# Optimization experiments

Hardware: AMD Instinct MI355X
Metric: run time of the kernel (lower is better)

The kernel has to match this reference:

```python
import jax, jax.numpy as jnp
import numpy as np

NEG = -100000000.0  # NOT_POSSIBLE_TRANSITION
B, T, F, NT = 64, 512, 1024, 50
H = NT + 2  # +2 for start/stop tags
START, STOP = H - 2, H - 1


def setup_inputs() -> dict:
    key = jax.random.key(0)
    k0, k1, k2, k3 = jax.random.split(key, 4)
    features = jax.random.normal(k0, (B, T, F), jnp.float32)
    tags = jax.random.randint(k1, (B, T), 0, NT)
    masks = jnp.ones((B, T), jnp.float32)
    W = jax.random.normal(k2, (H, F), jnp.float32) * 0.02  # nn.Linear weight
    b = jnp.zeros((H,), jnp.float32)                        # nn.Linear bias
    transition = jax.random.normal(k3, (H, H), jnp.float32)
    transition = transition.at[START, :].set(NEG).at[:, STOP].set(NEG)
    return dict(features=features, W=W, b=b, transition=transition,
                masks=masks, tags=tags)


def _forward_algorithm(emit, masks, transition):
    # emit: [B,T,H], masks: [B,T]
    b_, _, h = emit.shape
    init = jnp.full((b_, h), NEG, emit.dtype).at[:, START].set(0.0)

    def step(scores, xs):
        emit_t, mask_t = xs  # [B,H], [B]
        # score_t[b, i] = logsumexp_j(scores[b,j] + transition[i,j] + emit_t[b,i])
        s = scores[:, None, :] + transition[None, :, :] + emit_t[:, :, None]
        s = jax.nn.logsumexp(s, axis=-1)
        m = mask_t[:, None]
        scores = s * m + scores * (1.0 - m)
        return scores, None

    scores, _ = jax.lax.scan(step, init, (emit.transpose(1, 0, 2), masks.T))
    return jax.nn.logsumexp(scores + transition[STOP], axis=-1)  # [B]


def _gold_score(emit, tags, masks, transition):
    b_ = emit.shape[0]
    emit_sc = jnp.take_along_axis(emit, tags[:, :, None], axis=2)[:, :, 0]  # [B,T]
    start = jnp.full((b_, 1), START, tags.dtype)
    tags_ext = jnp.concatenate([start, tags], axis=1)  # [B,T+1]
    trans_sc = transition[tags_ext[:, 1:], tags_ext[:, :-1]]  # [B,T]
    last_pos = masks.sum(axis=1).astype(jnp.int32)  # index into tags_ext
    last_tag = jnp.take_along_axis(tags_ext, last_pos[:, None], axis=1)[:, 0]
    last_score = transition[STOP, last_tag]
    return ((trans_sc + emit_sc) * masks).sum(axis=1) + last_score  # [B]


def reference(features, W, b, transition, masks, tags):
    emit = features @ W.T + b  # [B,T,H]
    fwd = _forward_algorithm(emit, masks, transition)
    gold = _gold_score(emit, tags, masks, transition)
    return (fwd - gold).mean()  # CRF NLL loss (scalar)


if __name__ == "__main__":
    print(reference(**setup_inputs()))
```

## Files before the change

### kernel.cpp

```cpp
#include <hip/hip_runtime.h>
#include <hip/hip_bf16.h>
#include <math.h>


#define NEGV   (-100000000.0f)
#define BB     64
#define TT     512
#define FF     1024
#define HH     52
#define HP     64
#define S_START 50
#define S_STOP  51
#define NCHUNK 8
#define CLEN   (TT / NCHUNK)

typedef __bf16 bf16x8 __attribute__((ext_vector_type(8)));
typedef __bf16 bf16x4 __attribute__((ext_vector_type(4)));
typedef float  f32x4  __attribute__((ext_vector_type(4)));

#define WS_EMIT   0u
#define WS_CHUNK  8388608u
#define WS_WBF    16777216u
#define WS_GOLD   16908288u
#define WS_CEXP   16908544u

__global__ __launch_bounds__(256) void k_prep(const float* __restrict__ W,
                                              __bf16* __restrict__ wbf) {
  int n = blockIdx.x;
  for (int k = threadIdx.x; k < FF; k += 256) {
    float v = (n < HH) ? W[n * FF + k] : 0.0f;
    wbf[n * FF + k] = (__bf16)v;
  }
}

__global__ __launch_bounds__(256) void k_emit(const float* __restrict__ feat,
                                              const __bf16* __restrict__ wbf,
                                              const float* __restrict__ bias,
                                              float* __restrict__ emit) {
  __shared__ __align__(16) __bf16 Asm[64 * 72];
  const int tid = threadIdx.x;
  const int wv = tid >> 6;
  const int l  = tid & 63;
  const int lm = l & 15;
  const int q  = l >> 4;
  const size_t row0 = (size_t)blockIdx.x * 64;

  float bn[4];
#pragma unroll
  for (int nt = 0; nt < 4; ++nt) {
    int n = nt * 16 + lm;
    bn[nt] = (n < HH) ? bias[n] : 0.0f;
  }

  f32x4 acc[4] = {};

  const int srow = tid >> 4;
  const int scol = (tid & 15) * 4;

  for (int kc = 0; kc < 16; ++kc) {
    const int k0 = kc * 64;
    if (kc) __syncthreads();
#pragma unroll
    for (int p = 0; p < 4; ++p) {
      int r = srow + p * 16;
      f32x4 v = *(const f32x4*)(feat + (row0 + r) * FF + k0 + scol);
      bf16x4 bv;
#pragma unroll
      for (int j = 0; j < 4; ++j) bv[j] = (__bf16)v[j];
      *(bf16x4*)&Asm[r * 72 + scol] = bv;
    }
    __syncthreads();
#pragma unroll
    for (int kk = 0; kk < 2; ++kk) {
      bf16x8 af = *(const bf16x8*)&Asm[(wv * 16 + lm) * 72 + kk * 32 + q * 8];
#pragma unroll
      for (int nt = 0; nt < 4; ++nt) {
        bf16x8 bfr = *(const bf16x8*)(wbf + (size_t)(nt * 16 + lm) * FF + k0 + kk * 32 + q * 8);
        acc[nt] = __builtin_amdgcn_mfma_f32_16x16x32_bf16(af, bfr, acc[nt], 0, 0, 0);
      }
    }
  }

#pragma unroll
  for (int nt = 0; nt < 4; ++nt) {
#pragma unroll
    for (int rr = 0; rr < 4; ++rr) {
      size_t m = row0 + wv * 16 + q * 4 + rr;
      emit[m * HP + nt * 16 + lm] = acc[nt][rr] + bn[nt];
    }
  }
}

__global__ __launch_bounds__(256) void k_gold(const float* __restrict__ emit,
                                              const int* __restrict__ tags,
                                              const float* __restrict__ masks,
                                              const float* __restrict__ trans,
                                              float* __restrict__ gold) {
  const int b = blockIdx.x;
  const int tid = threadIdx.x;
  float acc = 0.f, msum = 0.f;
  for (int t = tid; t < TT; t += 256) {
    int tg = tags[b * TT + t];
    int pv = (t == 0) ? S_START : tags[b * TT + t - 1];
    float m = masks[b * TT + t];
    float e = emit[((size_t)b * TT + t) * HP + tg];
    float tr = trans[tg * HH + pv];
    acc += (e + tr) * m;
    msum += m;
  }
#pragma unroll
  for (int d = 32; d > 0; d >>= 1) {
    acc += __shfl_xor(acc, d);
    msum += __shfl_xor(msum, d);
  }
  __shared__ float ra[4], rm[4];
  if ((tid & 63) == 0) { ra[tid >> 6] = acc; rm[tid >> 6] = msum; }
  __syncthreads();
  if (tid == 0) {
    float tot = ra[0] + ra[1] + ra[2] + ra[3];
    float ms  = rm[0] + rm[1] + rm[2] + rm[3];
    int lp = (int)(ms + 0.5f);
    int lt = (lp == 0) ? S_START : tags[b * TT + lp - 1];
    gold[b] = tot + trans[S_STOP * HH + lt];
  }
}

__global__ __launch_bounds__(256) void k_chunks(const float* __restrict__ emit,
                                                const float* __restrict__ trans,
                                                const float* __restrict__ masks,
                                                float* __restrict__ chunks,
                                                float* __restrict__ cexp) {
  const int blk = blockIdx.x;
  const int b = blk >> 3, c = blk & 7;
  const int tid = threadIdx.x;
  const int wv = tid >> 6;
  const int l = tid & 63;
  const int lm = l & 15;
  const int q = l >> 4;

  __shared__ __align__(16) __bf16 PT[2][64 * 72];
  __shared__ float wmax[2][4];

  const int m = wv * 16 + lm;
  bf16x8 afrag[2];
#pragma unroll
  for (int kk = 0; kk < 2; ++kk) {
#pragma unroll
    for (int j = 0; j < 8; ++j) {
      int k = kk * 32 + q * 8 + j;
      float tv;
      if (k >= HH) tv = NEGV;
      else if (m >= HH) tv = 0.0f;
      else tv = trans[m * HH + k];
      afrag[kk][j] = (__bf16)__expf(tv);
    }
  }

  for (int idx = tid; idx < 4096; idx += 256) {
    int n = idx >> 6, mm = idx & 63;
    PT[0][n * 72 + mm] = (__bf16)((n == mm) ? 1.0f : 0.0f);
  }
  if (tid < 4) wmax[0][tid] = 1.0f;
  __syncthreads();

  const float* eb = emit + ((size_t)b * TT + c * CLEN) * HP + wv * 16 + q * 4;
  const float* mb = masks + b * TT + c * CLEN;
  f32x4 epf = *(const f32x4*)(eb);
  float mpf = mb[0];

  int pb = 0;
  int eacc = 0;

  for (int t = 0; t < CLEN; ++t) {
    f32x4 ecur = epf;
    float mcur = mpf;
    int tn = (t + 1 < CLEN) ? t + 1 : t;
    epf = *(const f32x4*)(eb + (size_t)tn * HP);
    mpf = mb[tn];

    if (mcur != 0.0f) {
      float pm = fmaxf(fmaxf(wmax[pb][0], wmax[pb][1]),
                       fmaxf(wmax[pb][2], wmax[pb][3]));
      int r = ilogbf(pm);
      const int nb = pb ^ 1;

      f32x4 acc[4] = {};
#pragma unroll
      for (int kk = 0; kk < 2; ++kk) {
#pragma unroll
        for (int nt = 0; nt < 4; ++nt) {
          bf16x8 bfr = *(const bf16x8*)&PT[pb][(nt * 16 + lm) * 72 + kk * 32 + q * 8];
          acc[nt] = __builtin_amdgcn_mfma_f32_16x16x32_bf16(afrag[kk], bfr, acc[nt], 0, 0, 0);
        }
      }
      float s[4];
#pragma unroll
      for (int rr = 0; rr < 4; ++rr) s[rr] = ldexpf(__expf(ecur[rr]), -r);

      float mx = 0.0f;
#pragma unroll
      for (int nt = 0; nt < 4; ++nt) {
        bf16x4 w4;
#pragma unroll
        for (int rr = 0; rr < 4; ++rr) {
          float v = acc[nt][rr] * s[rr];
          mx = fmaxf(mx, v);
          w4[rr] = (__bf16)v;
        }
        *(bf16x4*)&PT[nb][(nt * 16 + lm) * 72 + wv * 16 + q * 4] = w4;
      }
#pragma unroll
      for (int d = 1; d < 64; d <<= 1) mx = fmaxf(mx, __shfl_xor(mx, d));
      if (l == 0) wmax[nb][wv] = mx;
      eacc += r;
      __syncthreads();
      pb = nb;
    }
  }

  for (int idx = tid; idx < 4096; idx += 256) {
    int i = idx >> 6, j = idx & 63;
    chunks[(size_t)blk * 4096 + idx] = (float)PT[pb][j * 72 + i];
  }
  if (tid == 0) cexp[blk] = (float)eacc;
}

__global__ __launch_bounds__(64) void k_combine(const float* __restrict__ chunks,
                                                const float* __restrict__ cexp,
                                                const float* __restrict__ trans,
                                                const float* __restrict__ gold,
                                                float* __restrict__ out) {
  const int b = blockIdx.x;
  const int l = threadIdx.x;
  __shared__ float vsh[64];
  float v = (l == S_START) ? 1.0f : 0.0f;
  float esum = 0.0f;
  const float LN2 = 0.6931471805599453f;

  for (int cc = 0; cc < NCHUNK; ++cc) {
    vsh[l] = v;
    __syncthreads();
    const f32x4* Mr = (const f32x4*)(chunks + ((size_t)b * NCHUNK + cc) * 4096 + l * 64);
    float u = 0.0f;
#pragma unroll
    for (int jj = 0; jj < 16; ++jj) {
      f32x4 mv = Mr[jj];
      u += mv[0] * vsh[jj * 4 + 0] + mv[1] * vsh[jj * 4 + 1] +
           mv[2] * vsh[jj * 4 + 2] + mv[3] * vsh[jj * 4 + 3];
    }
    esum += cexp[b * NCHUNK + cc] * LN2;
    float mxx = u;
#pragma unroll
    for (int d = 1; d < 64; d <<= 1) mxx = fmaxf(mxx, __shfl_xor(mxx, d));
    if (mxx > 0.0f) {
      int ee = ilogbf(mxx);
      u = ldexpf(u, -ee);
      esum += (float)ee * LN2;
    }
    v = u;
    __syncthreads();
  }

  float ts = (l < HH) ? trans[S_STOP * HH + l] : NEGV;
  float contrib = v * __expf(ts);
#pragma unroll
  for (int d = 1; d < 64; d <<= 1) contrib += __shfl_xor(contrib, d);
  if (l == 0) {
    float fwd = __logf(contrib) + esum;
    atomicAdd(out, (fwd - gold[b]) * (1.0f / 64.0f));
  }
}

extern "C" void kernel_launch(void* const* d_in, const int* in_sizes, int n_in,
                              void* d_out, int out_size, void* d_ws, size_t ws_size,
                              hipStream_t stream) {
  (void)in_sizes; (void)n_in; (void)out_size; (void)ws_size;
  const float* feat  = (const float*)d_in[0];
  const float* W     = (const float*)d_in[1];
  const float* bias  = (const float*)d_in[2];
  const float* trans = (const float*)d_in[3];
  const float* masks = (const float*)d_in[4];
  const int*   tags  = (const int*)d_in[5];

  char* ws = (char*)d_ws;
  float*  emit   = (float*)(ws + WS_EMIT);
  float*  chunks = (float*)(ws + WS_CHUNK);
  __bf16* wbf    = (__bf16*)(ws + WS_WBF);
  float*  gold   = (float*)(ws + WS_GOLD);
  float*  cexp   = (float*)(ws + WS_CEXP);

  hipMemsetAsync(d_out, 0, sizeof(float), stream);
  k_prep<<<HP, 256, 0, stream>>>(W, wbf);
  k_emit<<<(BB * TT) / 64, 256, 0, stream>>>(feat, wbf, bias, emit);
  k_gold<<<BB, 256, 0, stream>>>(emit, tags, masks, trans, gold);
  k_chunks<<<BB * NCHUNK, 256, 0, stream>>>(emit, trans, masks, chunks, cexp);
  k_combine<<<BB, 64, 0, stream>>>(chunks, cexp, trans, gold, (float*)d_out);
}
```

Measured before the change: 298.6 us.

## Run one CRF chunk per wavefront with fixed rescaling and register-staged emit GEMM

The chunked forward-algorithm kernel now gives each wavefront a whole 64x64 chunk product, with sixteen chunks per sequence instead of eight. This removes the per-step block barrier and the shared-memory max exchange. Rescaling uses a fixed shift plus a max check every eight steps, so the cross-wave reduction no longer runs on every step. The emission GEMM loads features straight into registers with a one-step prefetch instead of staging them through LDS, and the combine kernel reads chunk matrices in a coalesced layout. The risks are bf16 overflow or underflow between the sparse rescale checks, higher register pressure, and more chunk data to combine.

```diff
diff --git a/kernel.cpp b/kernel.cpp
--- a/kernel.cpp
+++ b/kernel.cpp
@@ -11,8 +11,8 @@
 #define HP     64
 #define S_START 50
 #define S_STOP  51
-#define NCHUNK 8
-#define CLEN   (TT / NCHUNK)
+#define NCH    16
+#define CLEN   (TT / NCH)
 
 typedef __bf16 bf16x8 __attribute__((ext_vector_type(8)));
 typedef __bf16 bf16x4 __attribute__((ext_vector_type(4)));
@@ -20,9 +20,9 @@
 
 #define WS_EMIT   0u
 #define WS_CHUNK  8388608u
-#define WS_WBF    16777216u
-#define WS_GOLD   16908288u
-#define WS_CEXP   16908544u
+#define WS_WBF    25165824u
+#define WS_GOLD   25296896u
+#define WS_CEXP   25297152u
 
 __global__ __launch_bounds__(256) void k_prep(const float* __restrict__ W,
                                               __bf16* __restrict__ wbf) {
@@ -37,13 +37,13 @@
                                               const __bf16* __restrict__ wbf,
                                               const float* __restrict__ bias,
                                               float* __restrict__ emit) {
-  __shared__ __align__(16) __bf16 Asm[64 * 72];
   const int tid = threadIdx.x;
   const int wv = tid >> 6;
   const int l  = tid & 63;
   const int lm = l & 15;
   const int q  = l >> 4;
   const size_t row0 = (size_t)blockIdx.x * 64;
+  const float* fr = feat + (row0 + wv * 16 + lm) * FF;
 
   float bn[4];
 #pragma unroll
@@ -54,31 +54,44 @@
 
   f32x4 acc[4] = {};
 
-  const int srow = tid >> 4;
-  const int scol = (tid & 15) * 4;
+  f32x4 xa[2][2];
+#pragma unroll
+  for (int kk = 0; kk < 2; ++kk)
+#pragma unroll
+    for (int h = 0; h < 2; ++h)
+      xa[kk][h] = *(const f32x4*)(fr + kk * 32 + q * 8 + h * 4);
 
   for (int kc = 0; kc < 16; ++kc) {
+    bf16x8 af[2];
+#pragma unroll
+    for (int kk = 0; kk < 2; ++kk)
+#pragma unroll
+      for (int j = 0; j < 4; ++j) {
+        af[kk][j]     = (__bf16)xa[kk][0][j];
+        af[kk][4 + j] = (__bf16)xa[kk][1][j];
+      }
+    f32x4 xn[2][2];
+    if (kc < 15) {
+      const float* nf = fr + (kc + 1) * 64;
+#pragma unroll
+      for (int kk = 0; kk < 2; ++kk)
+#pragma unroll
+        for (int h = 0; h < 2; ++h)
+          xn[kk][h] = *(const f32x4*)(nf + kk * 32 + q * 8 + h * 4);
+    }
     const int k0 = kc * 64;
-    if (kc) __syncthreads();
-#pragma unroll
-    for (int p = 0; p < 4; ++p) {
-      int r = srow + p * 16;
-      f32x4 v = *(const f32x4*)(feat + (row0 + r) * FF + k0 + scol);
-      bf16x4 bv;
-#pragma unroll
-      for (int j = 0; j < 4; ++j) bv[j] = (__bf16)v[j];
-      *(bf16x4*)&Asm[r * 72 + scol] = bv;
-    }
-    __syncthreads();
-#pragma unroll
-    for (int kk = 0; kk < 2; ++kk) {
-      bf16x8 af = *(const bf16x8*)&Asm[(wv * 16 + lm) * 72 + kk * 32 + q * 8];
+#pragma unroll
+    for (int kk = 0; kk < 2; ++kk)
 #pragma unroll
       for (int nt = 0; nt < 4; ++nt) {
         bf16x8 bfr = *(const bf16x8*)(wbf + (size_t)(nt * 16 + lm) * FF + k0 + kk * 32 + q * 8);
-        acc[nt] = __builtin_amdgcn_mfma_f32_16x16x32_bf16(af, bfr, acc[nt], 0, 0, 0);
-      }
-    }
+        acc[nt] = __builtin_amdgcn_mfma_f32_16x16x32_bf16(af[kk], bfr, acc[nt], 0, 0, 0);
+      }
+#pragma unroll
+    for (int kk = 0; kk < 2; ++kk)
+#pragma unroll
+      for (int h = 0; h < 2; ++h)
+        xa[kk][h] = xn[kk][h];
   }
 
 #pragma unroll
@@ -125,104 +138,111 @@
   }
 }
 
-__global__ __launch_bounds__(256) void k_chunks(const float* __restrict__ emit,
-                                                const float* __restrict__ trans,
-                                                const float* __restrict__ masks,
-                                                float* __restrict__ chunks,
-                                                float* __restrict__ cexp) {
-  const int blk = blockIdx.x;
-  const int b = blk >> 3, c = blk & 7;
+__global__ __launch_bounds__(256, 1) void k_chunks(const float* __restrict__ emit,
+                                                   const float* __restrict__ trans,
+                                                   const float* __restrict__ masks,
+                                                   float* __restrict__ chunks,
+                                                   float* __restrict__ cexp) {
   const int tid = threadIdx.x;
   const int wv = tid >> 6;
-  const int l = tid & 63;
+  const int l  = tid & 63;
   const int lm = l & 15;
-  const int q = l >> 4;
-
-  __shared__ __align__(16) __bf16 PT[2][64 * 72];
-  __shared__ float wmax[2][4];
-
-  const int m = wv * 16 + lm;
-  bf16x8 afrag[2];
-#pragma unroll
-  for (int kk = 0; kk < 2; ++kk) {
-#pragma unroll
-    for (int j = 0; j < 8; ++j) {
-      int k = kk * 32 + q * 8 + j;
-      float tv;
-      if (k >= HH) tv = NEGV;
-      else if (m >= HH) tv = 0.0f;
-      else tv = trans[m * HH + k];
-      afrag[kk][j] = (__bf16)__expf(tv);
-    }
-  }
-
-  for (int idx = tid; idx < 4096; idx += 256) {
+  const int q  = l >> 4;
+  const int chunk = blockIdx.x * 4 + wv;
+  const int b = chunk >> 4, c = chunk & 15;
+
+  __shared__ __align__(16) __bf16 PTall[4][64 * 72];
+  __bf16* pt = PTall[wv];
+
+  bf16x8 afrag[4][2];
+#pragma unroll
+  for (int mt = 0; mt < 4; ++mt)
+#pragma unroll
+    for (int kk = 0; kk < 2; ++kk)
+#pragma unroll
+      for (int j = 0; j < 8; ++j) {
+        int m = mt * 16 + lm, k = kk * 32 + q * 8 + j;
+        float tv = (k >= HH) ? NEGV : ((m >= HH) ? 0.0f : trans[m * HH + k]);
+        afrag[mt][kk][j] = (__bf16)__expf(tv);
+      }
+
+  for (int idx = l; idx < 4096; idx += 64) {
     int n = idx >> 6, mm = idx & 63;
-    PT[0][n * 72 + mm] = (__bf16)((n == mm) ? 1.0f : 0.0f);
-  }
-  if (tid < 4) wmax[0][tid] = 1.0f;
-  __syncthreads();
-
-  const float* eb = emit + ((size_t)b * TT + c * CLEN) * HP + wv * 16 + q * 4;
+    pt[n * 72 + mm] = (__bf16)((n == mm) ? 1.0f : 0.0f);
+  }
+
+  const float* eb = emit + ((size_t)(b * TT + c * CLEN)) * HP;
   const float* mb = masks + b * TT + c * CLEN;
-  f32x4 epf = *(const f32x4*)(eb);
+
+  f32x4 ep[4];
+#pragma unroll
+  for (int mt = 0; mt < 4; ++mt) ep[mt] = *(const f32x4*)(eb + mt * 16 + q * 4);
   float mpf = mb[0];
 
-  int pb = 0;
-  int eacc = 0;
+  int eacc = 0, rpend = 0;
+  const float LOG2E = 1.4426950408889634f;
 
   for (int t = 0; t < CLEN; ++t) {
-    f32x4 ecur = epf;
+    f32x4 ec[4];
+#pragma unroll
+    for (int mt = 0; mt < 4; ++mt) ec[mt] = ep[mt];
     float mcur = mpf;
     int tn = (t + 1 < CLEN) ? t + 1 : t;
-    epf = *(const f32x4*)(eb + (size_t)tn * HP);
+#pragma unroll
+    for (int mt = 0; mt < 4; ++mt)
+      ep[mt] = *(const f32x4*)(eb + (size_t)tn * HP + mt * 16 + q * 4);
     mpf = mb[tn];
 
     if (mcur != 0.0f) {
-      float pm = fmaxf(fmaxf(wmax[pb][0], wmax[pb][1]),
-                       fmaxf(wmax[pb][2], wmax[pb][3]));
-      int r = ilogbf(pm);
-      const int nb = pb ^ 1;
-
-      f32x4 acc[4] = {};
-#pragma unroll
-      for (int kk = 0; kk < 2; ++kk) {
+      float sh = (float)(7 + rpend);
+      eacc += 7 + rpend;
+      rpend = 0;
+      float s[4][4];
+#pragma unroll
+      for (int mt = 0; mt < 4; ++mt)
+#pragma unroll
+        for (int rr = 0; rr < 4; ++rr)
+          s[mt][rr] = __builtin_amdgcn_exp2f(fmaf(ec[mt][rr], LOG2E, -sh));
+
+      bf16x8 bfr[2][4];
+#pragma unroll
+      for (int kk = 0; kk < 2; ++kk)
+#pragma unroll
+        for (int nt = 0; nt < 4; ++nt)
+          bfr[kk][nt] = *(const bf16x8*)&pt[(nt * 16 + lm) * 72 + kk * 32 + q * 8];
+
+      const bool trk = ((t & 7) == 7) && (t != CLEN - 1);
+      float lmax = 0.0f;
+      f32x4 zero = {};
+#pragma unroll
+      for (int mt = 0; mt < 4; ++mt) {
 #pragma unroll
         for (int nt = 0; nt < 4; ++nt) {
-          bf16x8 bfr = *(const bf16x8*)&PT[pb][(nt * 16 + lm) * 72 + kk * 32 + q * 8];
-          acc[nt] = __builtin_amdgcn_mfma_f32_16x16x32_bf16(afrag[kk], bfr, acc[nt], 0, 0, 0);
+          f32x4 a = __builtin_amdgcn_mfma_f32_16x16x32_bf16(afrag[mt][0], bfr[0][nt], zero, 0, 0, 0);
+          a = __builtin_amdgcn_mfma_f32_16x16x32_bf16(afrag[mt][1], bfr[1][nt], a, 0, 0, 0);
+          bf16x4 w4;
+#pragma unroll
+          for (int rr = 0; rr < 4; ++rr) {
+            float v = a[rr] * s[mt][rr];
+            if (trk) lmax = fmaxf(lmax, v);
+            w4[rr] = (__bf16)v;
+          }
+          *(bf16x4*)&pt[(nt * 16 + lm) * 72 + mt * 16 + q * 4] = w4;
         }
       }
-      float s[4];
-#pragma unroll
-      for (int rr = 0; rr < 4; ++rr) s[rr] = ldexpf(__expf(ecur[rr]), -r);
-
-      float mx = 0.0f;
-#pragma unroll
-      for (int nt = 0; nt < 4; ++nt) {
-        bf16x4 w4;
-#pragma unroll
-        for (int rr = 0; rr < 4; ++rr) {
-          float v = acc[nt][rr] * s[rr];
-          mx = fmaxf(mx, v);
-          w4[rr] = (__bf16)v;
-        }
-        *(bf16x4*)&PT[nb][(nt * 16 + lm) * 72 + wv * 16 + q * 4] = w4;
-      }
-#pragma unroll
-      for (int d = 1; d < 64; d <<= 1) mx = fmaxf(mx, __shfl_xor(mx, d));
-      if (l == 0) wmax[nb][wv] = mx;
-      eacc += r;
-      __syncthreads();
-      pb = nb;
-    }
-  }
-
-  for (int idx = tid; idx < 4096; idx += 256) {
-    int i = idx >> 6, j = idx & 63;
-    chunks[(size_t)blk * 4096 + idx] = (float)PT[pb][j * 72 + i];
-  }
-  if (tid == 0) cexp[blk] = (float)eacc;
+      if (trk) {
+#pragma unroll
+        for (int d = 1; d < 64; d <<= 1) lmax = fmaxf(lmax, __shfl_xor(lmax, d));
+        rpend = ilogbf(lmax);
+      }
+    }
+  }
+
+  for (int idx = l; idx < 4096; idx += 64) {
+    int jj = idx >> 8, i = (idx >> 2) & 63, jr = idx & 3;
+    chunks[(size_t)chunk * 4096 + idx] = (float)pt[(jj * 4 + jr) * 72 + i];
+  }
+  if (l == 0) cexp[chunk] = (float)eacc;
 }
 
 __global__ __launch_bounds__(64) void k_combine(const float* __restrict__ chunks,
@@ -237,18 +257,22 @@
   float esum = 0.0f;
   const float LN2 = 0.6931471805599453f;
 
-  for (int cc = 0; cc < NCHUNK; ++cc) {
+  for (int cc = 0; cc < NCH; ++cc) {
     vsh[l] = v;
     __syncthreads();
-    const f32x4* Mr = (const f32x4*)(chunks + ((size_t)b * NCHUNK + cc) * 4096 + l * 64);
-    float u = 0.0f;
+    const f32x4* M = (const f32x4*)(chunks + ((size_t)(b * NCH + cc)) * 4096);
+    f32x4 u4 = {};
 #pragma unroll
     for (int jj = 0; jj < 16; ++jj) {
-      f32x4 mv = Mr[jj];
-      u += mv[0] * vsh[jj * 4 + 0] + mv[1] * vsh[jj * 4 + 1] +
-           mv[2] * vsh[jj * 4 + 2] + mv[3] * vsh[jj * 4 + 3];
-    }
-    esum += cexp[b * NCHUNK + cc] * LN2;
+      f32x4 m4 = M[jj * 64 + l];
+      const float* vj = &vsh[jj * 4];
+      u4[0] += m4[0] * vj[0];
+      u4[1] += m4[1] * vj[1];
+      u4[2] += m4[2] * vj[2];
+      u4[3] += m4[3] * vj[3];
+    }
+    float u = (u4[0] + u4[1]) + (u4[2] + u4[3]);
+    esum += cexp[b * NCH + cc] * LN2;
     float mxx = u;
 #pragma unroll
     for (int d = 1; d < 64; d <<= 1) mxx = fmaxf(mxx, __shfl_xor(mxx, d));
@@ -293,6 +317,6 @@
   k_prep<<<HP, 256, 0, stream>>>(W, wbf);
   k_emit<<<(BB * TT) / 64, 256, 0, stream>>>(feat, wbf, bias, emit);
   k_gold<<<BB, 256, 0, stream>>>(emit, tags, masks, trans, gold);
-  k_chunks<<<BB * NCHUNK, 256, 0, stream>>>(emit, trans, masks, chunks, cexp);
+  k_chunks<<<(BB * NCH) / 4, 256, 0, stream>>>(emit, trans, masks, chunks, cexp);
   k_combine<<<BB, 64, 0, stream>>>(chunks, cexp, trans, gold, (float*)d_out);
 }
```

Measured after the change: 280.9 us. -5.9%, faster.
